# Performance work log

Measured on AMD Instinct MI355X. Metric: run time of the kernel, lower is better.

Reference implementation:

```python
import jax, jax.numpy as jnp
import numpy as np

D_MODEL = 1024
NUM_HEADS = 16
HEAD_DIM = D_MODEL // NUM_HEADS


def setup_inputs() -> dict:
    key = jax.random.key(0)
    ks = jax.random.split(key, 5)
    s = 1.0 / np.sqrt(D_MODEL)
    return {
        "x": jax.random.normal(ks[0], (2, 2048, D_MODEL), dtype=jnp.float32),
        "Wqkv": jax.random.normal(ks[1], (3 * D_MODEL, D_MODEL), dtype=jnp.float32) * s,
        "bqkv": jax.random.normal(ks[2], (3 * D_MODEL,), dtype=jnp.float32) * s,
        "Wo": jax.random.normal(ks[3], (D_MODEL, D_MODEL), dtype=jnp.float32) * s,
        "bo": jax.random.normal(ks[4], (D_MODEL,), dtype=jnp.float32) * s,
    }


def reference(x, Wqkv, bqkv, Wo, bo):
    B, S, D = x.shape
    H, hd = NUM_HEADS, HEAD_DIM
    # fused QKV projection (torch Linear: x @ W.T + b)
    qkv = x @ Wqkv.T + bqkv                      # [B, S, 3D]
    qkv = qkv.reshape(B, S, H, 3 * hd).transpose(0, 2, 1, 3)  # [B, H, S, 3hd]
    q, k, v = jnp.split(qkv, 3, axis=-1)         # each [B, H, S, hd]
    scaled = jnp.einsum("bhqd,bhkd->bhqk", q, k) / jnp.sqrt(jnp.float32(hd))
    # module applies causal mask when its `mask` flag is False (the default)
    causal = jnp.tril(jnp.ones((S, S), dtype=bool))
    scaled = jnp.where(causal, scaled, -jnp.inf)
    attn = jax.nn.softmax(scaled, axis=-1)       # [B, H, S, S]
    values = jnp.einsum("bhqk,bhkd->bhqd", attn, v)  # [B, H, S, hd]
    # NOTE: original uses .reshape (not transpose-then-reshape) on the
    # [B, H, S, hd] tensor directly — reproduce that exact layout.
    values = values.reshape(B, S, H * hd)
    out = values @ Wo.T + bo                     # [B, S, D]
    return out
```

## Files before the change

kernel.cpp:

```cpp
#include <hip/hip_runtime.h>

typedef __attribute__((ext_vector_type(8))) short bf16x8;
typedef __attribute__((ext_vector_type(4))) float f32x4;

#define D_MODEL 1024
#define NHEADS 16
#define HDIM 64
#define SEQ 2048
#define BATCH 2
#define MROWS (BATCH*SEQ)
#define NQKV (3*D_MODEL)
#define QSCALE 0.1803368801111204f
#define LPAD 72
#define CSTR 144

__device__ __forceinline__ unsigned short f2bf(float f) {
  unsigned int u = __float_as_uint(f);
  u += 0x7FFF + ((u >> 16) & 1);
  return (unsigned short)(u >> 16);
}
__device__ __forceinline__ unsigned int pack2bf(float a, float b) {
#if __has_builtin(__builtin_amdgcn_cvt_pk_bf16_f32)
  auto r = __builtin_amdgcn_cvt_pk_bf16_f32(a, b);
  unsigned int u; __builtin_memcpy(&u, &r, 4);
  return u;
#else
  return ((unsigned int)f2bf(b) << 16) | (unsigned int)f2bf(a);
#endif
}

__device__ __forceinline__ void gload16(const void* g, void* l) {
  __builtin_amdgcn_global_load_lds((const __attribute__((address_space(1))) void*)g,
                                   (__attribute__((address_space(3))) void*)l, 16, 0, 0);
}

#define N4_X     1048576
#define N4_WQKV   786432
#define N4_WO     262144
__global__ void cvt_all_kernel(const float4* __restrict__ x,
                               const float4* __restrict__ wqkv,
                               const float4* __restrict__ wo,
                               ushort4* __restrict__ xb,
                               ushort4* __restrict__ wqkvb,
                               ushort4* __restrict__ wob) {
  int i = blockIdx.x * blockDim.x + threadIdx.x;
  const float4* s; ushort4* d; int j;
  if (i < N4_X)                { s = x;    d = xb;    j = i; }
  else if (i < N4_X + N4_WQKV) { s = wqkv; d = wqkvb; j = i - N4_X; }
  else                         { s = wo;   d = wob;   j = i - (N4_X + N4_WQKV); }
  float4 v = s[j];
  ushort4 o;
  o.x = f2bf(v.x); o.y = f2bf(v.y); o.z = f2bf(v.z); o.w = f2bf(v.w);
  d[j] = o;
}

template<int MODE, int BM>
__global__ __launch_bounds__(256) void gemm_bt_kernel(
    const unsigned short* __restrict__ A,
    const unsigned short* __restrict__ Bm,
    const float* __restrict__ bias,
    float* __restrict__ outF,
    unsigned short* __restrict__ Qb,
    unsigned short* __restrict__ Kb,
    unsigned short* __restrict__ Vb,
    int M, int N, int K)
{
  constexpr int MI = BM / 32;
  constexpr int STG = BM*32 + 128*32;
  constexpr int SHSZ = (MODE == 0 && 128*CSTR > 2*STG) ? 128*CSTR : 2*STG;
  __shared__ __align__(16) unsigned short Sh[SHSZ];
  const int tid = threadIdx.x;
  const int wave = tid >> 6, lane = tid & 63;
  const int lm = lane & 15, quad = lane >> 4;
  const int wm = (wave >> 1) * (BM/2), wn = (wave & 1) * 64;
  const int m0 = blockIdx.y * BM, n0 = blockIdx.x * 128;

  f32x4 acc[MI][4] = {};

  auto stage_in = [&](int k0, int sb) {
    unsigned short* As = Sh + sb*STG;
    unsigned short* Bs = As + BM*32;
#pragma unroll
    for (int i = 0; i < BM/64; i++) {
      int ch = i*256 + tid;
      int r = ch >> 2, cg = (ch & 3) ^ ((r >> 1) & 3);
      gload16(&A[(size_t)(m0 + r) * K + k0 + cg*8], &As[ch*8]);
    }
#pragma unroll
    for (int i = 0; i < 2; i++) {
      int ch = i*256 + tid;
      int r = ch >> 2, cg = (ch & 3) ^ ((r >> 1) & 3);
      gload16(&Bm[(size_t)(n0 + r) * K + k0 + cg*8], &Bs[ch*8]);
    }
  };

  stage_in(0, 0);
  for (int k0 = 0; k0 < K; k0 += 32) {
    const int cur = (k0 >> 5) & 1;
    __syncthreads();
    if (k0 + 32 < K) stage_in(k0 + 32, cur ^ 1);
    const unsigned short* As = Sh + cur*STG;
    const unsigned short* Bs = As + BM*32;
    bf16x8 af[MI], bfr[4];
#pragma unroll
    for (int mi = 0; mi < MI; mi++) {
      int r = wm + mi*16 + lm;
      af[mi] = *(const bf16x8*)&As[(r*4 + (quad ^ ((r >> 1) & 3))) * 8];
    }
#pragma unroll
    for (int ni = 0; ni < 4; ni++) {
      int r = wn + ni*16 + lm;
      bfr[ni] = *(const bf16x8*)&Bs[(r*4 + (quad ^ ((r >> 1) & 3))) * 8];
    }
#pragma unroll
    for (int mi = 0; mi < MI; mi++)
#pragma unroll
      for (int ni = 0; ni < 4; ni++)
        acc[mi][ni] = __builtin_amdgcn_mfma_f32_16x16x32_bf16(af[mi], bfr[ni], acc[mi][ni], 0, 0, 0);
  }

  if (MODE == 1) {
#pragma unroll
    for (int mi = 0; mi < MI; mi++)
#pragma unroll
      for (int ni = 0; ni < 4; ni++)
#pragma unroll
        for (int r = 0; r < 4; r++) {
          int row = m0 + wm + mi*16 + quad*4 + r;
          int col = n0 + wn + ni*16 + lm;
          outF[(size_t)row * N + col] = acc[mi][ni][r] + bias[col];
        }
  } else {
    __syncthreads();
#pragma unroll
    for (int mi = 0; mi < MI; mi++)
#pragma unroll
      for (int ni = 0; ni < 4; ni++)
#pragma unroll
        for (int r = 0; r < 4; r++) {
          int row_l = wm + mi*16 + quad*4 + r;
          int col_l = wn + ni*16 + lm;
          int col = n0 + col_l;
          float v = acc[mi][ni][r] + bias[col];
          if (((col % 192) >> 6) == 0) v *= QSCALE;
          Sh[row_l*CSTR + col_l] = f2bf(v);
        }
    __syncthreads();
#pragma unroll
    for (int i = 0; i < BM*16/256; i++) {
      int lin = i*256 + tid;
      int row_l = lin >> 4, cc = (lin & 15) * 8;
      uint4 d = *(const uint4*)&Sh[row_l*CSTR + cc];
      int row = m0 + row_l, col = n0 + cc;
      int b = row >> 11, s = row & (SEQ - 1);
      int h = col / 192, rr = col - h*192;
      int ty = rr >> 6, e = rr & 63;
      size_t dsti = ((size_t)(b*NHEADS + h)*SEQ + s)*HDIM + e;
      unsigned short* dst = (ty == 0) ? Qb : (ty == 1) ? Kb : Vb;
      *(uint4*)&dst[dsti] = d;
    }
  }
}

__global__ __launch_bounds__(256) void vtrans_kernel(
    const unsigned short* __restrict__ Vb, unsigned short* __restrict__ VTb) {
  __shared__ __align__(16) unsigned short T[64*LPAD];
  const int bh = blockIdx.y, s0 = blockIdx.x * 64;
  const int tid = threadIdx.x;
#pragma unroll
  for (int i = 0; i < 2; i++) {
    int ch = i*256 + tid;
    int r = ch >> 3, c = (ch & 7) * 8;
    *(uint4*)&T[r*LPAD + c] = *(const uint4*)&Vb[((size_t)bh*SEQ + s0 + r)*HDIM + c];
  }
  __syncthreads();
#pragma unroll
  for (int i = 0; i < 2; i++) {
    int ch = i*256 + tid;
    int e = ch >> 3, c = (ch & 7) * 8;
    unsigned short tmp[8];
#pragma unroll
    for (int j = 0; j < 8; j++) tmp[j] = T[(c + j)*LPAD + e];
    *(uint4*)&VTb[((size_t)bh*HDIM + e)*SEQ + s0 + c] = *(const uint4*)tmp;
  }
}

__global__ __launch_bounds__(512) void flash_attn_kernel(
    const unsigned short* __restrict__ Qb,
    const unsigned short* __restrict__ Kb,
    const unsigned short* __restrict__ VTb,
    unsigned short* __restrict__ Ob)
{
  const int tid = threadIdx.x;
  const int wave = tid >> 6, lane = tid & 63;
  const int lm = lane & 15, quad = lane >> 4;
  const int lin = blockIdx.y * gridDim.x + blockIdx.x;
  const int xcd = lin & 7, j = lin >> 3;
  const int bh = xcd*4 + (j & 3);
  const int pr = j >> 2;
  const int t0 = 15 - pr, t1 = pr;
  const int nk0 = 2*(t0 + 1);
  const int ntot = nk0 + 2*(t1 + 1);

  __shared__ __align__(16) unsigned short Ks[2][64*64];
  __shared__ __align__(16) unsigned short Vs[2][64*64];
  __shared__ __align__(16) unsigned short Ps[8][16*64];

  const unsigned short* Qbh  = Qb  + (size_t)bh*SEQ*HDIM;
  const unsigned short* Kbh  = Kb  + (size_t)bh*SEQ*HDIM;
  const unsigned short* VTbh = VTb + (size_t)bh*HDIM*SEQ;
  unsigned short* Pw = &Ps[wave][lm * 64];
  const int sw = lm & 7;

  const int st_r = tid >> 3;
  const int st_cg = (tid & 7) ^ (st_r & 7);
  auto stage_in = [&](int k0, int sb) {
    gload16(&Kbh[(size_t)(k0 + st_r)*HDIM + st_cg*8], &Ks[sb][tid*8]);
    gload16(&VTbh[(size_t)st_r*SEQ + k0 + st_cg*8],   &Vs[sb][tid*8]);
  };

  int rowq = t0*128 + wave*16;
  int query = rowq + lm;
  bf16x8 qf[2];
#pragma unroll
  for (int kc = 0; kc < 2; kc++)
    qf[kc] = *(const bf16x8*)&Qbh[(size_t)query*HDIM + kc*32 + quad*8];

  f32x4 o[4] = {};
  float m_run = -1e30f, l_run = 0.f;

  stage_in(0, 0);
  for (int s = 0; s < ntot; s++) {
    const int kt = (s < nk0) ? s : s - nk0;
    const int k0 = kt * 64;
    const int cur = s & 1;
    __syncthreads();
    if (s + 1 < ntot) {
      int sn = s + 1;
      int ktn = (sn < nk0) ? sn : sn - nk0;
      stage_in(ktn * 64, cur ^ 1);
    }

    f32x4 sc[4] = {};
#pragma unroll
    for (int kc = 0; kc < 2; kc++)
#pragma unroll
      for (int mi = 0; mi < 4; mi++) {
        int r = mi*16 + lm, cc = kc*4 + quad;
        bf16x8 kf = *(const bf16x8*)&Ks[cur][(r*8 + (cc ^ (r & 7))) * 8];
        sc[mi] = __builtin_amdgcn_mfma_f32_16x16x32_bf16(kf, qf[kc], sc[mi], 0, 0, 0);
      }

    if (k0 + 63 > rowq) {
#pragma unroll
      for (int mi = 0; mi < 4; mi++)
#pragma unroll
        for (int r = 0; r < 4; r++) {
          int key = k0 + mi*16 + quad*4 + r;
          if (key > query) sc[mi][r] = -1e30f;
        }
    }

    float mx = sc[0][0];
#pragma unroll
    for (int mi = 0; mi < 4; mi++)
#pragma unroll
      for (int r = 0; r < 4; r++) mx = fmaxf(mx, sc[mi][r]);
    mx = fmaxf(mx, __shfl_xor(mx, 16, 64));
    mx = fmaxf(mx, __shfl_xor(mx, 32, 64));
    float mnew = fmaxf(m_run, mx);
    float alpha = exp2f(m_run - mnew);
    float p[4][4];
    float rs = 0.f;
#pragma unroll
    for (int mi = 0; mi < 4; mi++)
#pragma unroll
      for (int r = 0; r < 4; r++) {
        p[mi][r] = exp2f(sc[mi][r] - mnew);
        rs += p[mi][r];
      }
    rs += __shfl_xor(rs, 16, 64);
    rs += __shfl_xor(rs, 32, 64);
    l_run = l_run * alpha + rs;
    m_run = mnew;
#pragma unroll
    for (int ei = 0; ei < 4; ei++)
#pragma unroll
      for (int r = 0; r < 4; r++) o[ei][r] *= alpha;

#pragma unroll
    for (int mi = 0; mi < 4; mi++) {
      uint2 u;
      u.x = pack2bf(p[mi][0], p[mi][1]);
      u.y = pack2bf(p[mi][2], p[mi][3]);
      int chunk = (2*mi + (quad >> 1)) ^ sw;
      *(uint2*)&Pw[chunk*8 + (quad & 1)*4] = u;
    }
    asm volatile("s_waitcnt lgkmcnt(0)" ::: "memory");

#pragma unroll
    for (int kc = 0; kc < 2; kc++) {
      bf16x8 pf = *(const bf16x8*)&Pw[((kc*4 + quad) ^ sw) * 8];
#pragma unroll
      for (int ei = 0; ei < 4; ei++) {
        int e = ei*16 + lm, cc = kc*4 + quad;
        bf16x8 vf = *(const bf16x8*)&Vs[cur][(e*8 + (cc ^ (e & 7))) * 8];
        o[ei] = __builtin_amdgcn_mfma_f32_16x16x32_bf16(vf, pf, o[ei], 0, 0, 0);
      }
    }

    if (s == nk0 - 1 || s == ntot - 1) {
      float inv = 1.0f / l_run;
      size_t obase = ((size_t)bh*SEQ + query) * HDIM;
#pragma unroll
      for (int ei = 0; ei < 4; ei++) {
        uint2 u;
        u.x = pack2bf(o[ei][0]*inv, o[ei][1]*inv);
        u.y = pack2bf(o[ei][2]*inv, o[ei][3]*inv);
        *(uint2*)&Ob[obase + ei*16 + quad*4] = u;
      }
      if (s == nk0 - 1) {
        rowq = t1*128 + wave*16;
        query = rowq + lm;
#pragma unroll
        for (int kc = 0; kc < 2; kc++)
          qf[kc] = *(const bf16x8*)&Qbh[(size_t)query*HDIM + kc*32 + quad*8];
#pragma unroll
        for (int ei = 0; ei < 4; ei++)
#pragma unroll
          for (int r = 0; r < 4; r++) o[ei][r] = 0.f;
        m_run = -1e30f; l_run = 0.f;
      }
    }
  }
}

extern "C" void kernel_launch(void* const* d_in, const int* in_sizes, int n_in,
                              void* d_out, int out_size, void* d_ws, size_t ws_size,
                              hipStream_t stream) {
  const float* x    = (const float*)d_in[0];
  const float* Wqkv = (const float*)d_in[1];
  const float* bqkv = (const float*)d_in[2];
  const float* Wo   = (const float*)d_in[3];
  const float* bo   = (const float*)d_in[4];
  float* out = (float*)d_out;

  char* ws = (char*)d_ws;
  unsigned short* Xbf    = (unsigned short*)(ws);
  unsigned short* Wqkvbf = (unsigned short*)(ws + 8388608);
  unsigned short* Wobf   = (unsigned short*)(ws + 14680064);
  unsigned short* Qb     = (unsigned short*)(ws + 16777216);
  unsigned short* Kb     = (unsigned short*)(ws + 25165824);
  unsigned short* Vb     = (unsigned short*)(ws + 33554432);
  unsigned short* Ob     = (unsigned short*)(ws + 41943040);
  unsigned short* VTb    = Xbf;

  cvt_all_kernel<<<8192, 256, 0, stream>>>(
      (const float4*)x, (const float4*)Wqkv, (const float4*)Wo,
      (ushort4*)Xbf, (ushort4*)Wqkvbf, (ushort4*)Wobf);

  gemm_bt_kernel<0,128><<<dim3(24, 32), 256, 0, stream>>>(
      Xbf, Wqkvbf, bqkv, nullptr, Qb, Kb, Vb, MROWS, NQKV, D_MODEL);

  vtrans_kernel<<<dim3(32, 32), 256, 0, stream>>>(Vb, VTb);

  flash_attn_kernel<<<dim3(8, 32), 512, 0, stream>>>(Qb, Kb, VTb, Ob);

  gemm_bt_kernel<1,64><<<dim3(8, 64), 256, 0, stream>>>(
      Ob, Wobf, bo, out, nullptr, nullptr, nullptr, MROWS, D_MODEL, D_MODEL);
}
```

Measured before the change: 197.0 us.

## Replace paired causal tile scheduling with one query tile per block

```diff
diff --git a/kernel.cpp b/kernel.cpp
--- a/kernel.cpp
+++ b/kernel.cpp
@@ -194,13 +194,10 @@
   const int tid = threadIdx.x;
   const int wave = tid >> 6, lane = tid & 63;
   const int lm = lane & 15, quad = lane >> 4;
-  const int lin = blockIdx.y * gridDim.x + blockIdx.x;
-  const int xcd = lin & 7, j = lin >> 3;
-  const int bh = xcd*4 + (j & 3);
-  const int pr = j >> 2;
-  const int t0 = 15 - pr, t1 = pr;
-  const int nk0 = 2*(t0 + 1);
-  const int ntot = nk0 + 2*(t1 + 1);
+  const int bx = blockIdx.x;
+  const int bh = (bx & 7) * 4 + (bx >> 3);
+  const int t  = 15 - blockIdx.y;
+  const int nkt = 2 * (t + 1);
 
   __shared__ __align__(16) unsigned short Ks[2][64*64];
   __shared__ __align__(16) unsigned short Vs[2][64*64];
@@ -219,8 +216,8 @@
     gload16(&VTbh[(size_t)st_r*SEQ + k0 + st_cg*8],   &Vs[sb][tid*8]);
   };
 
-  int rowq = t0*128 + wave*16;
-  int query = rowq + lm;
+  const int rowq = t*128 + wave*16;
+  const int query = rowq + lm;
   bf16x8 qf[2];
 #pragma unroll
   for (int kc = 0; kc < 2; kc++)
@@ -230,16 +227,11 @@
   float m_run = -1e30f, l_run = 0.f;
 
   stage_in(0, 0);
-  for (int s = 0; s < ntot; s++) {
-    const int kt = (s < nk0) ? s : s - nk0;
-    const int k0 = kt * 64;
+  for (int s = 0; s < nkt; s++) {
+    const int k0 = s * 64;
     const int cur = s & 1;
     __syncthreads();
-    if (s + 1 < ntot) {
-      int sn = s + 1;
-      int ktn = (sn < nk0) ? sn : sn - nk0;
-      stage_in(ktn * 64, cur ^ 1);
-    }
+    if (s + 1 < nkt) stage_in(k0 + 64, cur ^ 1);
 
     f32x4 sc[4] = {};
 #pragma unroll
@@ -308,30 +300,16 @@
         o[ei] = __builtin_amdgcn_mfma_f32_16x16x32_bf16(vf, pf, o[ei], 0, 0, 0);
       }
     }
-
-    if (s == nk0 - 1 || s == ntot - 1) {
-      float inv = 1.0f / l_run;
-      size_t obase = ((size_t)bh*SEQ + query) * HDIM;
-#pragma unroll
-      for (int ei = 0; ei < 4; ei++) {
-        uint2 u;
-        u.x = pack2bf(o[ei][0]*inv, o[ei][1]*inv);
-        u.y = pack2bf(o[ei][2]*inv, o[ei][3]*inv);
-        *(uint2*)&Ob[obase + ei*16 + quad*4] = u;
-      }
-      if (s == nk0 - 1) {
-        rowq = t1*128 + wave*16;
-        query = rowq + lm;
-#pragma unroll
-        for (int kc = 0; kc < 2; kc++)
-          qf[kc] = *(const bf16x8*)&Qbh[(size_t)query*HDIM + kc*32 + quad*8];
-#pragma unroll
-        for (int ei = 0; ei < 4; ei++)
-#pragma unroll
-          for (int r = 0; r < 4; r++) o[ei][r] = 0.f;
-        m_run = -1e30f; l_run = 0.f;
-      }
-    }
+  }
+
+  float inv = 1.0f / l_run;
+  size_t obase = ((size_t)bh*SEQ + query) * HDIM;
+#pragma unroll
+  for (int ei = 0; ei < 4; ei++) {
+    uint2 u;
+    u.x = pack2bf(o[ei][0]*inv, o[ei][1]*inv);
+    u.y = pack2bf(o[ei][2]*inv, o[ei][3]*inv);
+    *(uint2*)&Ob[obase + ei*16 + quad*4] = u;
   }
 }
 
@@ -364,7 +342,7 @@
 
   vtrans_kernel<<<dim3(32, 32), 256, 0, stream>>>(Vb, VTb);
 
-  flash_attn_kernel<<<dim3(8, 32), 512, 0, stream>>>(Qb, Kb, VTb, Ob);
+  flash_attn_kernel<<<dim3(32, 16), 512, 0, stream>>>(Qb, Kb, VTb, Ob);
 
   gemm_bt_kernel<1,64><<<dim3(8, 64), 256, 0, stream>>>(
       Ob, Wobf, bo, out, nullptr, nullptr, nullptr, MROWS, D_MODEL, D_MODEL);
```

New measurement: 203.7 us. 3.4% more time.

## Fuse V transpose into QKV GEMM epilogue and widen attention key tiles

Applied to the files above, without the earlier changes.

```diff
diff --git a/kernel.cpp b/kernel.cpp
--- a/kernel.cpp
+++ b/kernel.cpp
@@ -11,7 +11,6 @@
 #define MROWS (BATCH*SEQ)
 #define NQKV (3*D_MODEL)
 #define QSCALE 0.1803368801111204f
-#define LPAD 72
 #define CSTR 144
 
 __device__ __forceinline__ unsigned short f2bf(float f) {
@@ -62,7 +61,7 @@
     float* __restrict__ outF,
     unsigned short* __restrict__ Qb,
     unsigned short* __restrict__ Kb,
-    unsigned short* __restrict__ Vb,
+    unsigned short* __restrict__ VTb,
     int M, int N, int K)
 {
   constexpr int MI = BM / 32;
@@ -147,41 +146,36 @@
         }
     __syncthreads();
 #pragma unroll
-    for (int i = 0; i < BM*16/256; i++) {
+    for (int i = 0; i < 8; i++) {
       int lin = i*256 + tid;
       int row_l = lin >> 4, cc = (lin & 15) * 8;
-      uint4 d = *(const uint4*)&Sh[row_l*CSTR + cc];
-      int row = m0 + row_l, col = n0 + cc;
-      int b = row >> 11, s = row & (SEQ - 1);
+      int col = n0 + cc;
       int h = col / 192, rr = col - h*192;
       int ty = rr >> 6, e = rr & 63;
-      size_t dsti = ((size_t)(b*NHEADS + h)*SEQ + s)*HDIM + e;
-      unsigned short* dst = (ty == 0) ? Qb : (ty == 1) ? Kb : Vb;
-      *(uint4*)&dst[dsti] = d;
-    }
-  }
-}
-
-__global__ __launch_bounds__(256) void vtrans_kernel(
-    const unsigned short* __restrict__ Vb, unsigned short* __restrict__ VTb) {
-  __shared__ __align__(16) unsigned short T[64*LPAD];
-  const int bh = blockIdx.y, s0 = blockIdx.x * 64;
-  const int tid = threadIdx.x;
-#pragma unroll
-  for (int i = 0; i < 2; i++) {
-    int ch = i*256 + tid;
-    int r = ch >> 3, c = (ch & 7) * 8;
-    *(uint4*)&T[r*LPAD + c] = *(const uint4*)&Vb[((size_t)bh*SEQ + s0 + r)*HDIM + c];
-  }
-  __syncthreads();
-#pragma unroll
-  for (int i = 0; i < 2; i++) {
-    int ch = i*256 + tid;
-    int e = ch >> 3, c = (ch & 7) * 8;
-    unsigned short tmp[8];
-#pragma unroll
-    for (int j = 0; j < 8; j++) tmp[j] = T[(c + j)*LPAD + e];
-    *(uint4*)&VTb[((size_t)bh*HDIM + e)*SEQ + s0 + c] = *(const uint4*)tmp;
+      if (ty < 2) {
+        uint4 d = *(const uint4*)&Sh[row_l*CSTR + cc];
+        int row = m0 + row_l;
+        int b = row >> 11, s = row & (SEQ - 1);
+        unsigned short* dst = ty ? Kb : Qb;
+        *(uint4*)&dst[((size_t)(b*NHEADS + h)*SEQ + s)*HDIM + e] = d;
+      }
+    }
+#pragma unroll
+    for (int i = 0; i < 8; i++) {
+      int lin = i*256 + tid;
+      int col_l = lin & 127, s8 = (lin >> 7) * 8;
+      int col = n0 + col_l;
+      int h = col / 192, rr = col - h*192;
+      if ((rr >> 6) == 2) {
+        int e = rr & 63;
+        unsigned short tmp[8];
+#pragma unroll
+        for (int j = 0; j < 8; j++) tmp[j] = Sh[(s8 + j)*CSTR + col_l];
+        int row = m0 + s8;
+        int b = row >> 11, s = row & (SEQ - 1);
+        *(uint4*)&VTb[((size_t)(b*NHEADS + h)*HDIM + e)*SEQ + s] = *(const uint4*)tmp;
+      }
+    }
   }
 }
 
@@ -194,29 +188,36 @@
   const int tid = threadIdx.x;
   const int wave = tid >> 6, lane = tid & 63;
   const int lm = lane & 15, quad = lane >> 4;
-  const int lin = blockIdx.y * gridDim.x + blockIdx.x;
-  const int xcd = lin & 7, j = lin >> 3;
-  const int bh = xcd*4 + (j & 3);
-  const int pr = j >> 2;
+  const int bx = blockIdx.x;
+  const int bh = (bx & 7) * 4 + (bx >> 3);
+  const int pr = blockIdx.y;
   const int t0 = 15 - pr, t1 = pr;
-  const int nk0 = 2*(t0 + 1);
-  const int ntot = nk0 + 2*(t1 + 1);
-
-  __shared__ __align__(16) unsigned short Ks[2][64*64];
-  __shared__ __align__(16) unsigned short Vs[2][64*64];
-  __shared__ __align__(16) unsigned short Ps[8][16*64];
+  const int nk0 = t0 + 1;
+  const int ntot = nk0 + t1 + 1;
+
+  __shared__ __align__(16) unsigned short Ks[2][128*64];
+  __shared__ __align__(16) unsigned short Vs[2][64*128];
+  __shared__ __align__(16) unsigned short Ps[8][16*128];
 
   const unsigned short* Qbh  = Qb  + (size_t)bh*SEQ*HDIM;
   const unsigned short* Kbh  = Kb  + (size_t)bh*SEQ*HDIM;
   const unsigned short* VTbh = VTb + (size_t)bh*HDIM*SEQ;
-  unsigned short* Pw = &Ps[wave][lm * 64];
+  unsigned short* Pw = &Ps[wave][lm * 128];
   const int sw = lm & 7;
 
-  const int st_r = tid >> 3;
-  const int st_cg = (tid & 7) ^ (st_r & 7);
   auto stage_in = [&](int k0, int sb) {
-    gload16(&Kbh[(size_t)(k0 + st_r)*HDIM + st_cg*8], &Ks[sb][tid*8]);
-    gload16(&VTbh[(size_t)st_r*SEQ + k0 + st_cg*8],   &Vs[sb][tid*8]);
+#pragma unroll
+    for (int i = 0; i < 2; i++) {
+      int ch = i*512 + tid;
+      int r = ch >> 3, cg = (ch & 7) ^ (r & 7);
+      gload16(&Kbh[(size_t)(k0 + r)*HDIM + cg*8], &Ks[sb][ch*8]);
+    }
+#pragma unroll
+    for (int i = 0; i < 2; i++) {
+      int ch = i*512 + tid;
+      int e = ch >> 4, cg = (ch & 15) ^ (e & 7);
+      gload16(&VTbh[(size_t)e*SEQ + k0 + cg*8], &Vs[sb][ch*8]);
+    }
   };
 
   int rowq = t0*128 + wave*16;
@@ -232,28 +233,28 @@
   stage_in(0, 0);
   for (int s = 0; s < ntot; s++) {
     const int kt = (s < nk0) ? s : s - nk0;
-    const int k0 = kt * 64;
+    const int k0 = kt * 128;
     const int cur = s & 1;
     __syncthreads();
     if (s + 1 < ntot) {
       int sn = s + 1;
       int ktn = (sn < nk0) ? sn : sn - nk0;
-      stage_in(ktn * 64, cur ^ 1);
-    }
-
-    f32x4 sc[4] = {};
+      stage_in(ktn * 128, cur ^ 1);
+    }
+
+    f32x4 sc[8] = {};
 #pragma unroll
     for (int kc = 0; kc < 2; kc++)
 #pragma unroll
-      for (int mi = 0; mi < 4; mi++) {
+      for (int mi = 0; mi < 8; mi++) {
         int r = mi*16 + lm, cc = kc*4 + quad;
         bf16x8 kf = *(const bf16x8*)&Ks[cur][(r*8 + (cc ^ (r & 7))) * 8];
         sc[mi] = __builtin_amdgcn_mfma_f32_16x16x32_bf16(kf, qf[kc], sc[mi], 0, 0, 0);
       }
 
-    if (k0 + 63 > rowq) {
-#pragma unroll
-      for (int mi = 0; mi < 4; mi++)
+    if (k0 + 127 > rowq) {
+#pragma unroll
+      for (int mi = 0; mi < 8; mi++)
 #pragma unroll
         for (int r = 0; r < 4; r++) {
           int key = k0 + mi*16 + quad*4 + r;
@@ -263,17 +264,17 @@
 
     float mx = sc[0][0];
 #pragma unroll
-    for (int mi = 0; mi < 4; mi++)
+    for (int mi = 0; mi < 8; mi++)
 #pragma unroll
       for (int r = 0; r < 4; r++) mx = fmaxf(mx, sc[mi][r]);
     mx = fmaxf(mx, __shfl_xor(mx, 16, 64));
     mx = fmaxf(mx, __shfl_xor(mx, 32, 64));
     float mnew = fmaxf(m_run, mx);
     float alpha = exp2f(m_run - mnew);
-    float p[4][4];
+    float p[8][4];
     float rs = 0.f;
 #pragma unroll
-    for (int mi = 0; mi < 4; mi++)
+    for (int mi = 0; mi < 8; mi++)
 #pragma unroll
       for (int r = 0; r < 4; r++) {
         p[mi][r] = exp2f(sc[mi][r] - mnew);
@@ -282,14 +283,16 @@
     rs += __shfl_xor(rs, 16, 64);
     rs += __shfl_xor(rs, 32, 64);
     l_run = l_run * alpha + rs;
+    if (__any(mnew != m_run)) {
+#pragma unroll
+      for (int ei = 0; ei < 4; ei++)
+#pragma unroll
+        for (int r = 0; r < 4; r++) o[ei][r] *= alpha;
+    }
     m_run = mnew;
-#pragma unroll
-    for (int ei = 0; ei < 4; ei++)
-#pragma unroll
-      for (int r = 0; r < 4; r++) o[ei][r] *= alpha;
-
-#pragma unroll
-    for (int mi = 0; mi < 4; mi++) {
+
+#pragma unroll
+    for (int mi = 0; mi < 8; mi++) {
       uint2 u;
       u.x = pack2bf(p[mi][0], p[mi][1]);
       u.y = pack2bf(p[mi][2], p[mi][3]);
@@ -299,12 +302,12 @@
     asm volatile("s_waitcnt lgkmcnt(0)" ::: "memory");
 
 #pragma unroll
-    for (int kc = 0; kc < 2; kc++) {
+    for (int kc = 0; kc < 4; kc++) {
       bf16x8 pf = *(const bf16x8*)&Pw[((kc*4 + quad) ^ sw) * 8];
 #pragma unroll
       for (int ei = 0; ei < 4; ei++) {
         int e = ei*16 + lm, cc = kc*4 + quad;
-        bf16x8 vf = *(const bf16x8*)&Vs[cur][(e*8 + (cc ^ (e & 7))) * 8];
+        bf16x8 vf = *(const bf16x8*)&Vs[cur][(e*16 + (cc ^ (e & 7))) * 8];
         o[ei] = __builtin_amdgcn_mfma_f32_16x16x32_bf16(vf, pf, o[ei], 0, 0, 0);
       }
     }
@@ -351,20 +354,17 @@
   unsigned short* Wobf   = (unsigned short*)(ws + 14680064);
   unsigned short* Qb     = (unsigned short*)(ws + 16777216);
   unsigned short* Kb     = (unsigned short*)(ws + 25165824);
-  unsigned short* Vb     = (unsigned short*)(ws + 33554432);
+  unsigned short* VTb    = (unsigned short*)(ws + 33554432);
   unsigned short* Ob     = (unsigned short*)(ws + 41943040);
-  unsigned short* VTb    = Xbf;
 
   cvt_all_kernel<<<8192, 256, 0, stream>>>(
       (const float4*)x, (const float4*)Wqkv, (const float4*)Wo,
       (ushort4*)Xbf, (ushort4*)Wqkvbf, (ushort4*)Wobf);
 
   gemm_bt_kernel<0,128><<<dim3(24, 32), 256, 0, stream>>>(
-      Xbf, Wqkvbf, bqkv, nullptr, Qb, Kb, Vb, MROWS, NQKV, D_MODEL);
-
-  vtrans_kernel<<<dim3(32, 32), 256, 0, stream>>>(Vb, VTb);
-
-  flash_attn_kernel<<<dim3(8, 32), 512, 0, stream>>>(Qb, Kb, VTb, Ob);
+      Xbf, Wqkvbf, bqkv, nullptr, Qb, Kb, VTb, MROWS, NQKV, D_MODEL);
+
+  flash_attn_kernel<<<dim3(32, 8), 512, 0, stream>>>(Qb, Kb, VTb, Ob);
 
   gemm_bt_kernel<1,64><<<dim3(8, 64), 256, 0, stream>>>(
       Ob, Wobf, bo, out, nullptr, nullptr, nullptr, MROWS, D_MODEL, D_MODEL);
```

Result: faster. 185.8 us (-5.7%).
